# Kernel tuning notes

Hardware: AMD Instinct MI355X
Metric: run time of the kernel (lower is better)

The kernel has to match this reference:

```python
import jax, jax.numpy as jnp
import numpy as np

L = 4      # num_gnn_layers
D = 128    # dim_latent
N = 50000  # nodes
E = 800000 # edges
BN_EPS = 1e-5


def setup_inputs() -> dict:
    key = jax.random.key(0)
    ks = jax.random.split(key, 16)
    w = lambda k: jax.random.normal(k, (L, D, D), jnp.float32) * 0.05
    b = lambda k: jax.random.normal(k, (L, D), jnp.float32) * 0.05
    return {
        "edge_index": jax.random.randint(ks[0], (2, E), 0, N, dtype=jnp.int64),
        "h": jax.random.normal(ks[1], (N, D), jnp.float32),
        "e": jax.random.normal(ks[2], (E, D), jnp.float32),
        "WA": w(ks[3]), "bA": b(ks[4]),
        "WB": w(ks[5]), "bB": b(ks[6]),
        "WC": w(ks[7]), "bC": b(ks[8]),
        "WU": w(ks[9]), "bU": b(ks[10]),
        "WVf": w(ks[11]), "bVf": b(ks[12]),
        "WVb": w(ks[13]), "bVb": b(ks[14]),
        "bnh_g": jnp.ones((L, D), jnp.float32), "bnh_b": jnp.zeros((L, D), jnp.float32),
        "bne_g": jnp.ones((L, D), jnp.float32), "bne_b": jnp.zeros((L, D), jnp.float32),
    }


def _bn(x, g, b):
    # BatchNorm1d, track_running_stats=False -> batch stats, biased variance
    mu = jnp.mean(x, axis=0)
    var = jnp.mean(jnp.square(x - mu), axis=0)
    return (x - mu) * jax.lax.rsqrt(var + BN_EPS) * g + b


def reference(edge_index, h, e,
              WA, bA, WB, bB, WC, bC, WU, bU, WVf, bVf, WVb, bVb,
              bnh_g, bnh_b, bne_g, bne_b):
    n = h.shape[0]
    s0, s1 = edge_index[0], edge_index[1]  # propagate always uses s0 -> s1

    for l in range(L):
        A = h @ WA[l].T + bA[l]
        B = h @ WB[l].T + bB[l]
        C = e @ WC[l].T + bC[l]
        U = h @ WU[l].T + bU[l]
        Vf = h @ WVf[l].T + bVf[l]
        Vb = h @ WVb[l].T + bVb[l]

        def gate(V, gsrc, gdst):
            ne = A[gsrc] + B[gdst] + C                      # [E, D]
            ne = jax.nn.relu(_bn(ne, bne_g[l], bne_b[l])) + e
            sig = jax.nn.sigmoid(ne)
            msg = V[s0] * sig / (sig + 1e-6)                # [E, D]
            agg = jax.ops.segment_sum(msg, s1, num_segments=n)
            return agg, ne

        h_f, e_f = gate(Vf, s0, s1)   # forward gate
        h_b, _ = gate(Vb, s1, s0)     # backward gate (A/B roles swapped only)

        h_new = jax.nn.relu(_bn(h_f + h_b + U, bnh_g[l], bnh_b[l])) + h
        h, e = h_new, e_f             # dropout is identity in eval

    return h, e
```

## Files before the change

### kernel.cpp

```cpp
#include <hip/hip_runtime.h>
#include <hip/hip_bf16.h>

#define N_NODES 50000
#define N_EDGES 800000
#define DIM 128
#define NLAYERS 4
#define BN_EPS 1e-5f
#define ECH 64

typedef unsigned short bf16_t;
typedef __attribute__((ext_vector_type(8))) short bf16x8;
typedef __attribute__((ext_vector_type(4))) float f32x4;

__device__ __forceinline__ float bf2f(bf16_t x) {
    unsigned int u = ((unsigned int)x) << 16;
    return __uint_as_float(u);
}
__device__ __forceinline__ bf16_t f2bf(float f) {
    unsigned int u = __float_as_uint(f);
    unsigned int r = (u + 0x7FFFu + ((u >> 16) & 1u)) >> 16;
    return (bf16_t)r;
}

__global__ __launch_bounds__(256) void hist_kernel(
    const int* __restrict__ s1, int* __restrict__ deg)
{
    int k = blockIdx.x * 256 + threadIdx.x;
    if (k < N_EDGES) atomicAdd(&deg[s1[k]], 1);
}

__global__ __launch_bounds__(1024) void scan_kernel(
    const int* __restrict__ deg, int* __restrict__ cursor)
{
    __shared__ int part[1024];
    const int t = threadIdx.x;
    const int CH = (N_NODES + 1023) / 1024;
    const int base = t * CH;
    int s = 0;
    for (int i = 0; i < CH; ++i) {
        int n = base + i;
        if (n < N_NODES) s += deg[n];
    }
    part[t] = s;
    __syncthreads();
    for (int off = 1; off < 1024; off <<= 1) {
        int v = (t >= off) ? part[t - off] : 0;
        __syncthreads();
        part[t] += v;
        __syncthreads();
    }
    int run = part[t] - s;
    for (int i = 0; i < CH; ++i) {
        int n = base + i;
        if (n < N_NODES) { cursor[n] = run; run += deg[n]; }
    }
}

__global__ __launch_bounds__(256) void scatter_kernel(
    const int* __restrict__ s0, const int* __restrict__ s1,
    int* __restrict__ cursor, int* __restrict__ perm,
    int* __restrict__ ssrc, int* __restrict__ sdst)
{
    int k = blockIdx.x * 256 + threadIdx.x;
    if (k < N_EDGES) {
        int d = s1[k];
        int pos = atomicAdd(&cursor[d], 1);
        perm[pos] = k;
        ssrc[pos] = s0[k];
        sdst[pos] = d;
    }
}

#define NG_TILE 64
#define NG_GRID ((N_NODES + NG_TILE - 1) / NG_TILE)

__global__ __launch_bounds__(256) void node_gemm_mfma(
    const float* __restrict__ h,
    const float* __restrict__ WA, const float* __restrict__ bA,
    const float* __restrict__ WB, const float* __restrict__ bB,
    const float* __restrict__ WU, const float* __restrict__ bU,
    const float* __restrict__ WVf, const float* __restrict__ bVf,
    const float* __restrict__ WVb, const float* __restrict__ bVb,
    bf16_t* __restrict__ A, bf16_t* __restrict__ B, bf16_t* __restrict__ U,
    bf16_t* __restrict__ Vf, bf16_t* __restrict__ Vb)
{
    __shared__ __align__(16) char hlds[NG_TILE * 256];

    const int tid  = threadIdx.x;
    const int lane = tid & 63;
    const int wv   = tid >> 6;
    const int l16  = lane & 15;
    const int lk   = lane >> 4;
    const long n0  = (long)blockIdx.x * NG_TILE;

    #pragma unroll
    for (int j = 0; j < 4; ++j) {
        const int idx = j * 256 + tid;
        const int row = idx >> 4, cb = idx & 15;
        long r = n0 + row;
        if (r >= N_NODES) r = N_NODES - 1;
        const float4* gp = (const float4*)(h + (size_t)r * DIM + cb * 8);
        float4 a = gp[0], b = gp[1];
        union { bf16x8 v; bf16_t s[8]; } u;
        u.s[0] = f2bf(a.x); u.s[1] = f2bf(a.y);
        u.s[2] = f2bf(a.z); u.s[3] = f2bf(a.w);
        u.s[4] = f2bf(b.x); u.s[5] = f2bf(b.y);
        u.s[6] = f2bf(b.z); u.s[7] = f2bf(b.w);
        const int off = row * 256 + ((cb * 16) ^ ((row & 7) << 4));
        *(bf16x8*)(&hlds[off]) = u.v;
    }
    __syncthreads();

    bf16x8 afrag[4][4];
    #pragma unroll
    for (int ks = 0; ks < 4; ++ks)
        #pragma unroll
        for (int mt = 0; mt < 4; ++mt) {
            const int row = mt * 16 + l16;
            const int off = row * 256 + ((ks * 64 + lk * 16) ^ ((row & 7) << 4));
            afrag[ks][mt] = *(const bf16x8*)(&hlds[off]);
        }

    const float* Ws[5] = {WA, WB, WU, WVf, WVb};
    const float* bs[5] = {bA, bB, bU, bVf, bVb};
    bf16_t* Os[5] = {A, B, U, Vf, Vb};

    #pragma unroll
    for (int m = 0; m < 5; ++m) {
        bf16x8 bfrag[2][4];
        float bias[2];
        #pragma unroll
        for (int nt = 0; nt < 2; ++nt) {
            const int n = wv * 32 + nt * 16 + l16;
            bias[nt] = bs[m][n];
            #pragma unroll
            for (int ks = 0; ks < 4; ++ks) {
                const int k = ks * 32 + lk * 8;
                const float4* wp = (const float4*)(Ws[m] + (size_t)n * DIM + k);
                float4 w0 = wp[0], w1 = wp[1];
                union { bf16x8 v; bf16_t s[8]; } u;
                u.s[0] = f2bf(w0.x); u.s[1] = f2bf(w0.y);
                u.s[2] = f2bf(w0.z); u.s[3] = f2bf(w0.w);
                u.s[4] = f2bf(w1.x); u.s[5] = f2bf(w1.y);
                u.s[6] = f2bf(w1.z); u.s[7] = f2bf(w1.w);
                bfrag[nt][ks] = u.v;
            }
        }

        f32x4 acc[4][2];
        #pragma unroll
        for (int mt = 0; mt < 4; ++mt)
            #pragma unroll
            for (int nt = 0; nt < 2; ++nt)
                acc[mt][nt] = (f32x4){0.f, 0.f, 0.f, 0.f};

        #pragma unroll
        for (int ks = 0; ks < 4; ++ks)
            #pragma unroll
            for (int mt = 0; mt < 4; ++mt)
                #pragma unroll
                for (int nt = 0; nt < 2; ++nt)
                    acc[mt][nt] = __builtin_amdgcn_mfma_f32_16x16x32_bf16(
                        afrag[ks][mt], bfrag[nt][ks], acc[mt][nt], 0, 0, 0);

        #pragma unroll
        for (int mt = 0; mt < 4; ++mt) {
            const long rbase = n0 + mt * 16 + lk * 4;
            #pragma unroll
            for (int nt = 0; nt < 2; ++nt) {
                const int col = wv * 32 + nt * 16 + l16;
                #pragma unroll
                for (int r = 0; r < 4; ++r) {
                    const long rr = rbase + r;
                    if (rr < N_NODES)
                        Os[m][rr * DIM + col] = f2bf(acc[mt][nt][r] + bias[nt]);
                }
            }
        }
    }
}

#define EG_TILE 64
#define EG_TILES 5
#define EG_GRID (N_EDGES / (EG_TILE * EG_TILES))

__global__ __launch_bounds__(256) void edge_gemm_mfma(
    const float* __restrict__ e, const float* __restrict__ WC,
    const float* __restrict__ bC, bf16_t* __restrict__ C)
{
    __shared__ __align__(16) char elds[2][EG_TILE * 256];

    const int tid  = threadIdx.x;
    const int lane = tid & 63;
    const int wv   = tid >> 6;
    const int l16  = lane & 15;
    const int lk   = lane >> 4;

    bf16x8 bfrag[2][4];
    float bias[2];
    #pragma unroll
    for (int nt = 0; nt < 2; ++nt) {
        const int n = wv * 32 + nt * 16 + l16;
        bias[nt] = bC[n];
        #pragma unroll
        for (int ks = 0; ks < 4; ++ks) {
            const int k = ks * 32 + lk * 8;
            const float4* wp = (const float4*)(WC + (size_t)n * DIM + k);
            float4 w0 = wp[0], w1 = wp[1];
            union { bf16x8 v; bf16_t s[8]; } u;
            u.s[0] = f2bf(w0.x); u.s[1] = f2bf(w0.y);
            u.s[2] = f2bf(w0.z); u.s[3] = f2bf(w0.w);
            u.s[4] = f2bf(w1.x); u.s[5] = f2bf(w1.y);
            u.s[6] = f2bf(w1.z); u.s[7] = f2bf(w1.w);
            bfrag[nt][ks] = u.v;
        }
    }

    float4 sreg[4][2];
    const long tile0 = (long)blockIdx.x * EG_TILES;

    auto load_tile = [&](long tile) {
        #pragma unroll
        for (int j = 0; j < 4; ++j) {
            const int idx = j * 256 + tid;
            const int row = idx >> 4, cb = idx & 15;
            const float4* gp = (const float4*)(
                e + (size_t)(tile * EG_TILE + row) * DIM + cb * 8);
            sreg[j][0] = gp[0]; sreg[j][1] = gp[1];
        }
    };
    auto write_lds = [&](int buf) {
        #pragma unroll
        for (int j = 0; j < 4; ++j) {
            const int idx = j * 256 + tid;
            const int row = idx >> 4, cb = idx & 15;
            union { bf16x8 v; bf16_t s[8]; } u;
            float4 a = sreg[j][0], b = sreg[j][1];
            u.s[0] = f2bf(a.x); u.s[1] = f2bf(a.y);
            u.s[2] = f2bf(a.z); u.s[3] = f2bf(a.w);
            u.s[4] = f2bf(b.x); u.s[5] = f2bf(b.y);
            u.s[6] = f2bf(b.z); u.s[7] = f2bf(b.w);
            const int off = row * 256 + ((cb * 16) ^ ((row & 7) << 4));
            *(bf16x8*)(&elds[buf][off]) = u.v;
        }
    };

    load_tile(tile0);
    write_lds(0);
    __syncthreads();
    int cur = 0;

    for (int t = 0; t < EG_TILES; ++t) {
        if (t + 1 < EG_TILES) load_tile(tile0 + t + 1);

        f32x4 acc[4][2];
        #pragma unroll
        for (int mt = 0; mt < 4; ++mt)
            #pragma unroll
            for (int nt = 0; nt < 2; ++nt)
                acc[mt][nt] = (f32x4){0.f, 0.f, 0.f, 0.f};

        #pragma unroll
        for (int ks = 0; ks < 4; ++ks) {
            bf16x8 afrag[4];
            #pragma unroll
            for (int mt = 0; mt < 4; ++mt) {
                const int row = mt * 16 + l16;
                const int off = row * 256 +
                    ((ks * 64 + lk * 16) ^ ((row & 7) << 4));
                afrag[mt] = *(const bf16x8*)(&elds[cur][off]);
            }
            #pragma unroll
            for (int mt = 0; mt < 4; ++mt)
                #pragma unroll
                for (int nt = 0; nt < 2; ++nt)
                    acc[mt][nt] = __builtin_amdgcn_mfma_f32_16x16x32_bf16(
                        afrag[mt], bfrag[nt][ks], acc[mt][nt], 0, 0, 0);
        }

        const long e0 = (tile0 + t) * EG_TILE;
        #pragma unroll
        for (int mt = 0; mt < 4; ++mt) {
            const long rbase = e0 + mt * 16 + lk * 4;
            #pragma unroll
            for (int nt = 0; nt < 2; ++nt) {
                const int col = wv * 32 + nt * 16 + l16;
                #pragma unroll
                for (int r = 0; r < 4; ++r)
                    C[(rbase + r) * DIM + col] = f2bf(acc[mt][nt][r] + bias[nt]);
            }
        }

        if (t + 1 < EG_TILES) {
            write_lds(cur ^ 1);
            __syncthreads();
            cur ^= 1;
        }
    }
}

__global__ __launch_bounds__(128) void edge_stats(
    const int* __restrict__ s0, const int* __restrict__ s1,
    const bf16_t* __restrict__ A, const bf16_t* __restrict__ B,
    const bf16_t* __restrict__ C, float* __restrict__ stats)
{
    __shared__ int ls0[ECH], ls1[ECH];
    const int t = threadIdx.x;
    const long k0 = (long)blockIdx.x * ECH;
    if (t < ECH) { ls0[t] = s0[k0 + t]; ls1[t] = s1[k0 + t]; }
    __syncthreads();

    float sf = 0.f, ssf = 0.f, sb = 0.f, ssb = 0.f;
    for (int i = 0; i < ECH; ++i) {
        const long k = k0 + i;
        const long a = ls0[i], b = ls1[i];
        float c  = bf2f(C[k * DIM + t]);
        float a0 = bf2f(A[a * DIM + t]);
        float b1 = bf2f(B[b * DIM + t]);
        float a1 = bf2f(A[b * DIM + t]);
        float b0 = bf2f(B[a * DIM + t]);
        float tf = a0 + b1 + c;
        float tb = a1 + b0 + c;
        sf += tf; ssf += tf * tf;
        sb += tb; ssb += tb * tb;
    }
    atomicAdd(&stats[t], sf);
    atomicAdd(&stats[128 + t], ssf);
    atomicAdd(&stats[256 + t], sb);
    atomicAdd(&stats[384 + t], ssb);
}

__global__ void finalize_edge_stats(float* __restrict__ stats)
{
    const int t = threadIdx.x;
    const float inv = 1.0f / (float)N_EDGES;
    if (t < 128) {
        float mu = stats[t] * inv;
        float var = stats[128 + t] * inv - mu * mu;
        stats[768 + t] = mu;
        stats[896 + t] = rsqrtf(var + BN_EPS);
    } else {
        int d = t - 128;
        float mu = stats[256 + d] * inv;
        float var = stats[384 + d] * inv - mu * mu;
        stats[1024 + d] = mu;
        stats[1152 + d] = rsqrtf(var + BN_EPS);
    }
}

__global__ __launch_bounds__(128) void edge_apply_sorted(
    const int* __restrict__ perm, const int* __restrict__ ssrc,
    const int* __restrict__ sdst,
    const bf16_t* __restrict__ A, const bf16_t* __restrict__ B,
    const bf16_t* __restrict__ C,
    const bf16_t* __restrict__ Vf, const bf16_t* __restrict__ Vb,
    const float* __restrict__ stats,
    const float* __restrict__ gne, const float* __restrict__ bne,
    float* __restrict__ ebuf, float* __restrict__ agg)
{
    __shared__ int lp[ECH], lsa[ECH], lsd[ECH];
    const int t = threadIdx.x;
    const long p0 = (long)blockIdx.x * ECH;
    if (t < ECH) {
        lp[t]  = perm[p0 + t];
        lsa[t] = ssrc[p0 + t];
        lsd[t] = sdst[p0 + t];
    }
    __syncthreads();

    const float g = gne[t], bb = bne[t];
    const float af = stats[896 + t] * g;
    const float cf = bb - stats[768 + t] * af;
    const float ab = stats[1152 + t] * g;
    const float cb = bb - stats[1024 + t] * ab;

    int cur = lsd[0];
    float Ad = bf2f(A[(long)cur * DIM + t]);
    float Bd = bf2f(B[(long)cur * DIM + t]);
    float acc = 0.f;

    for (int i = 0; i < ECH; ++i) {
        const int sd = lsd[i];
        if (sd != cur) {
            atomicAdd(&agg[(long)cur * DIM + t], acc);
            acc = 0.f;
            cur = sd;
            Ad = bf2f(A[(long)cur * DIM + t]);
            Bd = bf2f(B[(long)cur * DIM + t]);
        }
        const long k  = lp[i];
        const long sa = lsa[i];
        float c  = bf2f(C[k * DIM + t]);
        float a0 = bf2f(A[sa * DIM + t]);
        float b0 = bf2f(B[sa * DIM + t]);
        float ek = ebuf[k * DIM + t];

        float nf = fmaxf((a0 + Bd + c) * af + cf, 0.0f) + ek;
        float nb = fmaxf((Ad + b0 + c) * ab + cb, 0.0f) + ek;
        ebuf[k * DIM + t] = nf;

        float sigf = 1.0f / (1.0f + __expf(-nf));
        float sigb = 1.0f / (1.0f + __expf(-nb));
        float wf = sigf / (sigf + 1e-6f);
        float wb = sigb / (sigb + 1e-6f);
        acc += bf2f(Vf[sa * DIM + t]) * wf + bf2f(Vb[sa * DIM + t]) * wb;
    }
    atomicAdd(&agg[(long)cur * DIM + t], acc);
}

__global__ __launch_bounds__(128) void node_stats(
    const float* __restrict__ agg, const bf16_t* __restrict__ U,
    float* __restrict__ stats)
{
    const int t = threadIdx.x;
    const long n0 = (long)blockIdx.x * 50;
    float s = 0.f, ss = 0.f;
    for (int i = 0; i < 50; ++i) {
        const long n = n0 + i;
        float v = agg[n * DIM + t] + bf2f(U[n * DIM + t]);
        s += v; ss += v * v;
    }
    atomicAdd(&stats[512 + t], s);
    atomicAdd(&stats[640 + t], ss);
}

__global__ void finalize_node_stats(float* __restrict__ stats)
{
    const int t = threadIdx.x;
    const float inv = 1.0f / (float)N_NODES;
    float mu = stats[512 + t] * inv;
    float var = stats[640 + t] * inv - mu * mu;
    stats[1280 + t] = mu;
    stats[1408 + t] = rsqrtf(var + BN_EPS);
}

__global__ __launch_bounds__(256) void node_apply(
    const float* __restrict__ agg, const bf16_t* __restrict__ U,
    const float* __restrict__ stats,
    const float* __restrict__ gh, const float* __restrict__ bh,
    float* __restrict__ hbuf)
{
    const long i = (long)blockIdx.x * 256 + threadIdx.x;
    const int d = (int)(i & (DIM - 1));
    float v = agg[i] + bf2f(U[i]);
    float n = (v - stats[1280 + d]) * stats[1408 + d] * gh[d] + bh[d];
    hbuf[i] = fmaxf(n, 0.0f) + hbuf[i];
}

extern "C" void kernel_launch(void* const* d_in, const int* in_sizes, int n_in,
                              void* d_out, int out_size, void* d_ws, size_t ws_size,
                              hipStream_t stream)
{
    const int* ei = (const int*)d_in[0];
    const int* s0 = ei;
    const int* s1 = ei + N_EDGES;
    const float* h0 = (const float*)d_in[1];
    const float* e0 = (const float*)d_in[2];
    const float* WA = (const float*)d_in[3];  const float* bA = (const float*)d_in[4];
    const float* WB = (const float*)d_in[5];  const float* bB = (const float*)d_in[6];
    const float* WC = (const float*)d_in[7];  const float* bC = (const float*)d_in[8];
    const float* WU = (const float*)d_in[9];  const float* bU = (const float*)d_in[10];
    const float* WVf = (const float*)d_in[11]; const float* bVf = (const float*)d_in[12];
    const float* WVb = (const float*)d_in[13]; const float* bVb = (const float*)d_in[14];
    const float* bnh_g = (const float*)d_in[15]; const float* bnh_b = (const float*)d_in[16];
    const float* bne_g = (const float*)d_in[17]; const float* bne_b = (const float*)d_in[18];

    float* hbuf = (float*)d_out;
    float* ebuf = hbuf + (size_t)N_NODES * DIM;

    float* agg = (float*)d_ws;
    float* stats = agg + (size_t)N_NODES * DIM;
    bf16_t* Abuf  = (bf16_t*)(stats + 2048);
    bf16_t* Bbuf  = Abuf  + (size_t)N_NODES * DIM;
    bf16_t* Ubuf  = Bbuf  + (size_t)N_NODES * DIM;
    bf16_t* Vfbuf = Ubuf  + (size_t)N_NODES * DIM;
    bf16_t* Vbbuf = Vfbuf + (size_t)N_NODES * DIM;
    bf16_t* Cbuf  = Vbbuf + (size_t)N_NODES * DIM;
    int* deg    = (int*)(Cbuf + (size_t)N_EDGES * DIM);
    int* cursor = deg + N_NODES;
    int* perm   = cursor + N_NODES;
    int* ssrc   = perm + N_EDGES;
    int* sdst   = ssrc + N_EDGES;

    hipMemcpyAsync(hbuf, h0, (size_t)N_NODES * DIM * sizeof(float),
                   hipMemcpyDeviceToDevice, stream);
    hipMemcpyAsync(ebuf, e0, (size_t)N_EDGES * DIM * sizeof(float),
                   hipMemcpyDeviceToDevice, stream);

    hipMemsetAsync(deg, 0, N_NODES * sizeof(int), stream);
    hist_kernel<<<(N_EDGES + 255) / 256, 256, 0, stream>>>(s1, deg);
    scan_kernel<<<1, 1024, 0, stream>>>(deg, cursor);
    scatter_kernel<<<(N_EDGES + 255) / 256, 256, 0, stream>>>(
        s0, s1, cursor, perm, ssrc, sdst);

    for (int l = 0; l < NLAYERS; ++l) {
        const size_t wo = (size_t)l * DIM * DIM;
        const size_t bo = (size_t)l * DIM;
        hipMemsetAsync(agg, 0, ((size_t)N_NODES * DIM + 768) * sizeof(float), stream);

        node_gemm_mfma<<<NG_GRID, 256, 0, stream>>>(
            hbuf, WA + wo, bA + bo, WB + wo, bB + bo, WU + wo, bU + bo,
            WVf + wo, bVf + bo, WVb + wo, bVb + bo,
            Abuf, Bbuf, Ubuf, Vfbuf, Vbbuf);
        edge_gemm_mfma<<<EG_GRID, 256, 0, stream>>>(ebuf, WC + wo, bC + bo, Cbuf);
        edge_stats<<<N_EDGES / ECH, 128, 0, stream>>>(s0, s1, Abuf, Bbuf, Cbuf, stats);
        finalize_edge_stats<<<1, 256, 0, stream>>>(stats);
        edge_apply_sorted<<<N_EDGES / ECH, 128, 0, stream>>>(
            perm, ssrc, sdst, Abuf, Bbuf, Cbuf, Vfbuf, Vbbuf, stats,
            bne_g + bo, bne_b + bo, ebuf, agg);
        node_stats<<<N_NODES / 50, 128, 0, stream>>>(agg, Ubuf, stats);
        finalize_node_stats<<<1, 128, 0, stream>>>(stats);
        node_apply<<<(N_NODES * DIM) / 256, 256, 0, stream>>>(
            agg, Ubuf, stats, bnh_g + bo, bnh_b + bo, hbuf);
    }
}
```

Baseline: 4.601 ms.

## Interleave A/B and Vf/Vb node buffers and compute C in dst-sorted edge order

Node GEMM outputs are packed so A and B share one row of stride 256, and Vf and Vb share another. Gathers for the src and dst nodes then each touch one contiguous 512-byte row instead of two separate buffers. The edge GEMM reads e rows through perm, so C is laid out in dst-sorted order and edge_stats and edge_apply read C contiguously. In exchange, the random row gather moves from C reads to e reads inside the GEMM, and edge_apply now reloads the destination's A/B for every edge instead of caching them.

```diff
diff --git a/kernel.cpp b/kernel.cpp
--- a/kernel.cpp
+++ b/kernel.cpp
@@ -81,8 +81,7 @@
     const float* __restrict__ WU, const float* __restrict__ bU,
     const float* __restrict__ WVf, const float* __restrict__ bVf,
     const float* __restrict__ WVb, const float* __restrict__ bVb,
-    bf16_t* __restrict__ A, bf16_t* __restrict__ B, bf16_t* __restrict__ U,
-    bf16_t* __restrict__ Vf, bf16_t* __restrict__ Vb)
+    bf16_t* __restrict__ AB, bf16_t* __restrict__ U, bf16_t* __restrict__ V)
 {
     __shared__ __align__(16) char hlds[NG_TILE * 256];
 
@@ -123,7 +122,8 @@
 
     const float* Ws[5] = {WA, WB, WU, WVf, WVb};
     const float* bs[5] = {bA, bB, bU, bVf, bVb};
-    bf16_t* Os[5] = {A, B, U, Vf, Vb};
+    bf16_t* obase[5] = {AB, AB + 128, U, V, V + 128};
+    const long ostr[5] = {256, 256, 128, 256, 256};
 
     #pragma unroll
     for (int m = 0; m < 5; ++m) {
@@ -173,7 +173,7 @@
                 for (int r = 0; r < 4; ++r) {
                     const long rr = rbase + r;
                     if (rr < N_NODES)
-                        Os[m][rr * DIM + col] = f2bf(acc[mt][nt][r] + bias[nt]);
+                        obase[m][rr * ostr[m] + col] = f2bf(acc[mt][nt][r] + bias[nt]);
                 }
             }
         }
@@ -185,8 +185,9 @@
 #define EG_GRID (N_EDGES / (EG_TILE * EG_TILES))
 
 __global__ __launch_bounds__(256) void edge_gemm_mfma(
-    const float* __restrict__ e, const float* __restrict__ WC,
-    const float* __restrict__ bC, bf16_t* __restrict__ C)
+    const float* __restrict__ e, const int* __restrict__ perm,
+    const float* __restrict__ WC, const float* __restrict__ bC,
+    bf16_t* __restrict__ C)
 {
     __shared__ __align__(16) char elds[2][EG_TILE * 256];
 
@@ -224,8 +225,9 @@
         for (int j = 0; j < 4; ++j) {
             const int idx = j * 256 + tid;
             const int row = idx >> 4, cb = idx & 15;
+            const long gr = perm[tile * EG_TILE + row];
             const float4* gp = (const float4*)(
-                e + (size_t)(tile * EG_TILE + row) * DIM + cb * 8);
+                e + (size_t)gr * DIM + cb * 8);
             sreg[j][0] = gp[0]; sreg[j][1] = gp[1];
         }
     };
@@ -299,26 +301,26 @@
     }
 }
 
-__global__ __launch_bounds__(128) void edge_stats(
-    const int* __restrict__ s0, const int* __restrict__ s1,
-    const bf16_t* __restrict__ A, const bf16_t* __restrict__ B,
-    const bf16_t* __restrict__ C, float* __restrict__ stats)
-{
-    __shared__ int ls0[ECH], ls1[ECH];
+__global__ __launch_bounds__(128) void edge_stats_sorted(
+    const int* __restrict__ ssrc, const int* __restrict__ sdst,
+    const bf16_t* __restrict__ AB, const bf16_t* __restrict__ C,
+    float* __restrict__ stats)
+{
+    __shared__ int lsa[ECH], lsd[ECH];
     const int t = threadIdx.x;
     const long k0 = (long)blockIdx.x * ECH;
-    if (t < ECH) { ls0[t] = s0[k0 + t]; ls1[t] = s1[k0 + t]; }
+    if (t < ECH) { lsa[t] = ssrc[k0 + t]; lsd[t] = sdst[k0 + t]; }
     __syncthreads();
 
     float sf = 0.f, ssf = 0.f, sb = 0.f, ssb = 0.f;
+    #pragma unroll 4
     for (int i = 0; i < ECH; ++i) {
-        const long k = k0 + i;
-        const long a = ls0[i], b = ls1[i];
-        float c  = bf2f(C[k * DIM + t]);
-        float a0 = bf2f(A[a * DIM + t]);
-        float b1 = bf2f(B[b * DIM + t]);
-        float a1 = bf2f(A[b * DIM + t]);
-        float b0 = bf2f(B[a * DIM + t]);
+        const size_t sa = (size_t)lsa[i], sd = (size_t)lsd[i];
+        float a0 = bf2f(AB[sa * 256 + t]);
+        float b0 = bf2f(AB[sa * 256 + 128 + t]);
+        float a1 = bf2f(AB[sd * 256 + t]);
+        float b1 = bf2f(AB[sd * 256 + 128 + t]);
+        float c  = bf2f(C[(k0 + i) * DIM + t]);
         float tf = a0 + b1 + c;
         float tb = a1 + b0 + c;
         sf += tf; ssf += tf * tf;
@@ -351,9 +353,8 @@
 __global__ __launch_bounds__(128) void edge_apply_sorted(
     const int* __restrict__ perm, const int* __restrict__ ssrc,
     const int* __restrict__ sdst,
-    const bf16_t* __restrict__ A, const bf16_t* __restrict__ B,
-    const bf16_t* __restrict__ C,
-    const bf16_t* __restrict__ Vf, const bf16_t* __restrict__ Vb,
+    const bf16_t* __restrict__ AB, const bf16_t* __restrict__ C,
+    const bf16_t* __restrict__ V,
     const float* __restrict__ stats,
     const float* __restrict__ gne, const float* __restrict__ bne,
     float* __restrict__ ebuf, float* __restrict__ agg)
@@ -375,35 +376,33 @@
     const float cb = bb - stats[1024 + t] * ab;
 
     int cur = lsd[0];
-    float Ad = bf2f(A[(long)cur * DIM + t]);
-    float Bd = bf2f(B[(long)cur * DIM + t]);
     float acc = 0.f;
 
+    #pragma unroll 2
     for (int i = 0; i < ECH; ++i) {
         const int sd = lsd[i];
         if (sd != cur) {
             atomicAdd(&agg[(long)cur * DIM + t], acc);
             acc = 0.f;
             cur = sd;
-            Ad = bf2f(A[(long)cur * DIM + t]);
-            Bd = bf2f(B[(long)cur * DIM + t]);
-        }
-        const long k  = lp[i];
-        const long sa = lsa[i];
-        float c  = bf2f(C[k * DIM + t]);
-        float a0 = bf2f(A[sa * DIM + t]);
-        float b0 = bf2f(B[sa * DIM + t]);
+        }
+        const size_t k  = (size_t)lp[i];
+        const size_t sa = (size_t)lsa[i];
+        float a0 = bf2f(AB[sa * 256 + t]);
+        float b0 = bf2f(AB[sa * 256 + 128 + t]);
+        float a1 = bf2f(AB[(size_t)sd * 256 + t]);
+        float b1 = bf2f(AB[(size_t)sd * 256 + 128 + t]);
+        float c  = bf2f(C[(p0 + i) * DIM + t]);
         float ek = ebuf[k * DIM + t];
 
-        float nf = fmaxf((a0 + Bd + c) * af + cf, 0.0f) + ek;
-        float nb = fmaxf((Ad + b0 + c) * ab + cb, 0.0f) + ek;
+        float nf = fmaxf((a0 + b1 + c) * af + cf, 0.0f) + ek;
+        float nb = fmaxf((a1 + b0 + c) * ab + cb, 0.0f) + ek;
         ebuf[k * DIM + t] = nf;
 
         float sigf = 1.0f / (1.0f + __expf(-nf));
         float sigb = 1.0f / (1.0f + __expf(-nb));
-        float wf = sigf / (sigf + 1e-6f);
-        float wb = sigb / (sigb + 1e-6f);
-        acc += bf2f(Vf[sa * DIM + t]) * wf + bf2f(Vb[sa * DIM + t]) * wb;
+        acc += bf2f(V[sa * 256 + t]) * (sigf / (sigf + 1e-6f))
+             + bf2f(V[sa * 256 + 128 + t]) * (sigb / (sigb + 1e-6f));
     }
     atomicAdd(&agg[(long)cur * DIM + t], acc);
 }
@@ -470,12 +469,10 @@
 
     float* agg = (float*)d_ws;
     float* stats = agg + (size_t)N_NODES * DIM;
-    bf16_t* Abuf  = (bf16_t*)(stats + 2048);
-    bf16_t* Bbuf  = Abuf  + (size_t)N_NODES * DIM;
-    bf16_t* Ubuf  = Bbuf  + (size_t)N_NODES * DIM;
-    bf16_t* Vfbuf = Ubuf  + (size_t)N_NODES * DIM;
-    bf16_t* Vbbuf = Vfbuf + (size_t)N_NODES * DIM;
-    bf16_t* Cbuf  = Vbbuf + (size_t)N_NODES * DIM;
+    bf16_t* ABbuf = (bf16_t*)(stats + 2048);
+    bf16_t* Ubuf  = ABbuf + (size_t)N_NODES * 256;
+    bf16_t* Vbuf  = Ubuf  + (size_t)N_NODES * DIM;
+    bf16_t* Cbuf  = Vbuf  + (size_t)N_NODES * 256;
     int* deg    = (int*)(Cbuf + (size_t)N_EDGES * DIM);
     int* cursor = deg + N_NODES;
     int* perm   = cursor + N_NODES;
@@ -501,12 +498,14 @@
         node_gemm_mfma<<<NG_GRID, 256, 0, stream>>>(
             hbuf, WA + wo, bA + bo, WB + wo, bB + bo, WU + wo, bU + bo,
             WVf + wo, bVf + bo, WVb + wo, bVb + bo,
-            Abuf, Bbuf, Ubuf, Vfbuf, Vbbuf);
-        edge_gemm_mfma<<<EG_GRID, 256, 0, stream>>>(ebuf, WC + wo, bC + bo, Cbuf);
-        edge_stats<<<N_EDGES / ECH, 128, 0, stream>>>(s0, s1, Abuf, Bbuf, Cbuf, stats);
+            ABbuf, Ubuf, Vbuf);
+        edge_gemm_mfma<<<EG_GRID, 256, 0, stream>>>(
+            ebuf, perm, WC + wo, bC + bo, Cbuf);
+        edge_stats_sorted<<<N_EDGES / ECH, 128, 0, stream>>>(
+            ssrc, sdst, ABbuf, Cbuf, stats);
         finalize_edge_stats<<<1, 256, 0, stream>>>(stats);
         edge_apply_sorted<<<N_EDGES / ECH, 128, 0, stream>>>(
-            perm, ssrc, sdst, Abuf, Bbuf, Cbuf, Vfbuf, Vbbuf, stats,
+            perm, ssrc, sdst, ABbuf, Cbuf, Vbuf, stats,
             bne_g + bo, bne_b + bo, ebuf, agg);
         node_stats<<<N_NODES / 50, 128, 0, stream>>>(agg, Ubuf, stats);
         finalize_node_stats<<<1, 128, 0, stream>>>(stats);
```

Result: no change. 4.686 ms (+1.8%).
